# Optimization experiments

Hardware: AMD Instinct MI355X
Metric: run time of the kernel (lower is better)

## Reference

```python
import jax, jax.numpy as jnp
import numpy as np

HIDDEN = 1024
HEADS = 16
HEAD = HIDDEN // HEADS


def setup_inputs() -> dict:
    key = jax.random.key(0)
    ks = jax.random.split(key, 6)
    B, T = 2, 2048
    x = jax.random.normal(ks[0], (B, T, HIDDEN), dtype=jnp.float32)
    mask = jnp.ones((T, T), dtype=jnp.float32)
    s = 1.0 / np.sqrt(HIDDEN)
    Wqkv = jax.random.normal(ks[1], (HIDDEN, 3 * HIDDEN), dtype=jnp.float32) * s
    bqkv = jnp.zeros((3 * HIDDEN,), dtype=jnp.float32)
    Wproj = jax.random.normal(ks[2], (HIDDEN, HIDDEN), dtype=jnp.float32) * s
    bproj = jnp.zeros((HIDDEN,), dtype=jnp.float32)
    return {"x": x, "mask": mask, "Wqkv": Wqkv, "bqkv": bqkv,
            "Wproj": Wproj, "bproj": bproj}


def reference(x, mask, Wqkv, bqkv, Wproj, bproj):
    B, T, C = x.shape
    qkv = x @ Wqkv + bqkv                      # [B,T,3C]
    q, k, v = jnp.split(qkv, 3, axis=-1)
    def heads(t):                              # [B,T,C] -> [B,H,T,D]
        return t.reshape(B, T, HEADS, HEAD).transpose(0, 2, 1, 3)
    q, k, v = heads(q), heads(k), heads(v)
    scores = jnp.einsum('bhqd,bhkd->bhqk', q, k) / np.sqrt(HEAD)
    scores = jnp.where(mask == 0, -jnp.inf, scores)
    attn = jax.nn.softmax(scores, axis=-1)
    out = jnp.einsum('bhqk,bhkd->bhqd', attn, v)
    out = out.transpose(0, 2, 1, 3).reshape(B, T, C)
    return out @ Wproj + bproj
```

## Files before the change

kernel.cpp:

```cpp
#include <hip/hip_runtime.h>
#include <stdint.h>

#define HID 1024
#define NH 16
#define HD 64
#define BATCH 2
#define SEQ 2048
#define MR (BATCH*SEQ)
#define NQKV (3*HID)

typedef __attribute__((ext_vector_type(8))) _Float16 h16x8;
typedef __attribute__((ext_vector_type(2))) __fp16 fp16x2;
typedef __attribute__((ext_vector_type(8))) unsigned short u16x8;
typedef __attribute__((ext_vector_type(4))) float f32x4;

#if __has_builtin(__builtin_amdgcn_exp2f)
#define EXP2(x) __builtin_amdgcn_exp2f(x)
#else
#define EXP2(x) exp2f(x)
#endif

static __device__ __forceinline__ unsigned short f2h(float f) {
  union { _Float16 h; unsigned short u; } v; v.h = (_Float16)f; return v.u;
}
static __device__ __forceinline__ unsigned pk2(float a, float b) {
  union { fp16x2 h; unsigned u; } v;
  v.h = __builtin_amdgcn_cvt_pkrtz(a, b);
  return v.u;
}

typedef const __attribute__((address_space(1))) unsigned int glb_u32;
typedef __attribute__((address_space(3))) unsigned int lds_u32;
static __device__ __forceinline__ void cp16(const void* g, void* l) {
  __builtin_amdgcn_global_load_lds((glb_u32*)g, (lds_u32*)l, 16, 0, 0);
}

#define QSCL (0.125f * 1.44269504f)

__global__ __launch_bounds__(256) void k_cvt(const float4* __restrict__ src,
                                             ushort4* __restrict__ dst) {
  int i = blockIdx.x * 256 + threadIdx.x;
  float4 v = src[i];
  ushort4 h;
  h.x = f2h(v.x); h.y = f2h(v.y); h.z = f2h(v.z); h.w = f2h(v.w);
  dst[i] = h;
}

__global__ __launch_bounds__(256) void k_transpose_h(const float* __restrict__ src,
                                                     int R, int C,
                                                     unsigned short* __restrict__ dst) {
  __shared__ float tile[32][33];
  int tx = threadIdx.x, ty = threadIdx.y;
  int col0 = blockIdx.x * 32, row0 = blockIdx.y * 32;
  #pragma unroll
  for (int i = 0; i < 32; i += 8)
    tile[ty + i][tx] = src[(size_t)(row0 + ty + i) * C + col0 + tx];
  __syncthreads();
  #pragma unroll
  for (int i = 0; i < 32; i += 8) {
    float v = tile[tx][ty + i];
    dst[(size_t)(col0 + ty + i) * R + row0 + tx] = f2h(v);
  }
}

__global__ __launch_bounds__(256) void k_maskbits(const float* __restrict__ mask,
                                                  unsigned long long* __restrict__ mb) {
  int gw = blockIdx.x * 4 + (threadIdx.x >> 6);
  int lane = threadIdx.x & 63;
  float v = mask[(size_t)gw * 64 + lane];
  unsigned long long b = __ballot(v != 0.f);
  if (lane == 0) mb[gw] = b;
}

__global__ __launch_bounds__(256) void k_gemm_qkv(const unsigned short* __restrict__ A,
                                                  const unsigned short* __restrict__ Bt,
                                                  const float* __restrict__ bias,
                                                  unsigned short* __restrict__ Qp,
                                                  unsigned short* __restrict__ Kp,
                                                  unsigned short* __restrict__ Vt) {
  const int K = HID;
  int tid = threadIdx.x;
  int wave = tid >> 6, lane = tid & 63, quad = lane >> 4, l16 = lane & 15;
  int wm = wave >> 1, wn = wave & 1;
  int x7 = l16 & 7;
  int m0 = blockIdx.y * 128, n0 = blockIdx.x * 128;
  __shared__ __align__(16) unsigned short As[128 * 64], Bs[128 * 64];
  f32x4 acc[4][4] = {};
  for (int k0 = 0; k0 < K; k0 += 64) {
    __syncthreads();
    #pragma unroll
    for (int i = 0; i < 4; i++) {
      int c = tid + i * 256;
      int r = c >> 3, sc = ((c ^ r) & 7) << 3;
      cp16(&A[(size_t)(m0 + r) * K + k0 + sc], &As[c << 3]);
      cp16(&Bt[(size_t)(n0 + r) * K + k0 + sc], &Bs[c << 3]);
    }
    __syncthreads();
    #pragma unroll
    for (int kc = 0; kc < 2; kc++) {
      h16x8 af[4], bf[4];
      #pragma unroll
      for (int i = 0; i < 4; i++) {
        af[i] = *(const h16x8*)&As[(wm * 64 + i * 16 + l16) * 64 + (((kc * 4 + quad) ^ x7) << 3)];
        bf[i] = *(const h16x8*)&Bs[(wn * 64 + i * 16 + l16) * 64 + (((kc * 4 + quad) ^ x7) << 3)];
      }
      #pragma unroll
      for (int i = 0; i < 4; i++)
        #pragma unroll
        for (int j = 0; j < 4; j++)
          acc[i][j] = __builtin_amdgcn_mfma_f32_16x16x32_f16(af[i], bf[j], acc[i][j], 0, 0, 0);
    }
  }
  #pragma unroll
  for (int j = 0; j < 4; j++) {
    int n = n0 + wn * 64 + j * 16 + l16;
    float bv = bias[n];
    int which = n >> 10;
    int rem = n & 1023;
    int h = rem >> 6, d = rem & 63;
    if (which == 2) {
      #pragma unroll
      for (int i = 0; i < 4; i++) {
        int m = m0 + wm * 64 + i * 16 + quad * 4;
        int b = m >> 11, t = m & 2047;
        uint2 tt;
        tt.x = pk2(acc[i][j][0] + bv, acc[i][j][1] + bv);
        tt.y = pk2(acc[i][j][2] + bv, acc[i][j][3] + bv);
        *(uint2*)&Vt[(size_t)(b * NH + h) * (SEQ * HD) + (size_t)d * SEQ + t] = tt;
      }
    } else {
      #pragma unroll
      for (int i = 0; i < 4; i++)
        #pragma unroll
        for (int r = 0; r < 4; r++) {
          int m = m0 + wm * 64 + i * 16 + quad * 4 + r;
          int b = m >> 11, t = m & 2047;
          float val = acc[i][j][r] + bv;
          int hb = b * NH + h;
          if (which == 0) Qp[(size_t)hb * (SEQ * HD) + (size_t)t * HD + d] = f2h(val * QSCL);
          else            Kp[(size_t)hb * (SEQ * HD) + (size_t)t * HD + d] = f2h(val);
        }
    }
  }
}

__global__ __launch_bounds__(256) void k_attn(const unsigned short* __restrict__ Qp,
                                              const unsigned short* __restrict__ Kp,
                                              const unsigned short* __restrict__ Vt,
                                              const unsigned long long* __restrict__ mb,
                                              unsigned short* __restrict__ AO) {
  int tid = threadIdx.x, wave = tid >> 6, lane = tid & 63, quad = lane >> 4, l16 = lane & 15;
  int bh = blockIdx.y, qbase = blockIdx.x * 64;
  const unsigned short* Qg = Qp + (size_t)bh * (SEQ * HD);
  const unsigned short* Kg = Kp + (size_t)bh * (SEQ * HD);
  const unsigned short* Vg = Vt + (size_t)bh * (SEQ * HD);
  __shared__ __align__(16) unsigned short smem[16896];
  unsigned short* Qs = smem;
  unsigned short* Ks = smem + 4096;
  unsigned short* Vs = smem + 8192;
  unsigned short* Ps = smem + 12288 + wave * (16 * 72);
  unsigned short* Os = smem + 4096;

  #pragma unroll
  for (int i = 0; i < 2; i++) {
    int c = tid + i * 256;
    int row = c >> 3, sc = ((c ^ row) & 7) << 3;
    cp16(&Qg[(size_t)(qbase + row) * HD + sc], &Qs[c << 3]);
  }
  int qrow = qbase + wave * 16 + l16;
  const unsigned long long* mrow = mb + (size_t)qrow * 32;
  f32x4 acc_o[4] = {};
  f32x4 acc_l = {};
  int x7 = l16 & 7;

  h16x8 vone;
  #pragma unroll
  for (int j = 0; j < 8; j++) vone[j] = (_Float16)1.0f;

  __syncthreads();
  h16x8 bq[2];
  #pragma unroll
  for (int kk = 0; kk < 2; kk++)
    bq[kk] = *(const h16x8*)&Qs[(wave * 16 + l16) * 64 + (((kk * 4 + quad) ^ x7) << 3)];

  for (int kt = 0; kt < 32; kt++) {
    int kbase = kt * 64;
    __syncthreads();
    #pragma unroll
    for (int i = 0; i < 2; i++) {
      int c = tid + i * 256;
      int row = c >> 3, sc = ((c ^ row) & 7) << 3;
      cp16(&Kg[(size_t)(kbase + row) * HD + sc], &Ks[c << 3]);
      cp16(&Vg[(size_t)row * SEQ + kbase + sc], &Vs[c << 3]);
    }
    unsigned long long w = mrow[kt];
    __syncthreads();
    f32x4 s[4] = {};
    #pragma unroll
    for (int nt = 0; nt < 4; nt++)
      #pragma unroll
      for (int kk = 0; kk < 2; kk++) {
        h16x8 a = *(const h16x8*)&Ks[(nt * 16 + l16) * 64 + (((kk * 4 + quad) ^ x7) << 3)];
        s[nt] = __builtin_amdgcn_mfma_f32_16x16x32_f16(a, bq[kk], s[nt], 0, 0, 0);
      }
    if (!__all(w == ~0ULL)) {
      #pragma unroll
      for (int nt = 0; nt < 4; nt++)
        #pragma unroll
        for (int r = 0; r < 4; r++)
          if (!((w >> (nt * 16 + quad * 4 + r)) & 1ULL)) s[nt][r] = -100.f;
    }
    #pragma unroll
    for (int nt = 0; nt < 4; nt++)
      #pragma unroll
      for (int r = 0; r < 4; r++) s[nt][r] = EXP2(s[nt][r]);
    #pragma unroll
    for (int nt = 0; nt < 4; nt++) {
      uint2 t;
      t.x = pk2(s[nt][0], s[nt][1]);
      t.y = pk2(s[nt][2], s[nt][3]);
      *(uint2*)&Ps[l16 * 72 + nt * 16 + quad * 4] = t;
    }
    h16x8 bp[2];
    #pragma unroll
    for (int kk = 0; kk < 2; kk++)
      bp[kk] = *(const h16x8*)&Ps[l16 * 72 + kk * 32 + quad * 8];
    acc_l = __builtin_amdgcn_mfma_f32_16x16x32_f16(vone, bp[0], acc_l, 0, 0, 0);
    acc_l = __builtin_amdgcn_mfma_f32_16x16x32_f16(vone, bp[1], acc_l, 0, 0, 0);
    #pragma unroll
    for (int nt = 0; nt < 4; nt++)
      #pragma unroll
      for (int kk = 0; kk < 2; kk++) {
        h16x8 a = *(const h16x8*)&Vs[(nt * 16 + l16) * 64 + (((kk * 4 + quad) ^ x7) << 3)];
        acc_o[nt] = __builtin_amdgcn_mfma_f32_16x16x32_f16(a, bp[kk], acc_o[nt], 0, 0, 0);
      }
  }
  float rl = 1.0f / acc_l[0];
  __syncthreads();
  #pragma unroll
  for (int nt = 0; nt < 4; nt++) {
    uint2 t;
    t.x = (unsigned)f2h(acc_o[nt][0] * rl) | ((unsigned)f2h(acc_o[nt][1] * rl) << 16);
    t.y = (unsigned)f2h(acc_o[nt][2] * rl) | ((unsigned)f2h(acc_o[nt][3] * rl) << 16);
    *(uint2*)&Os[(wave * 16 + l16) * 72 + nt * 16 + quad * 4] = t;
  }
  __syncthreads();
  int b = bh >> 4, h = bh & 15;
  #pragma unroll
  for (int i = 0; i < 2; i++) {
    int c = tid + i * 256;
    int row = c >> 3, co = (c & 7) << 3;
    u16x8 vv = *(const u16x8*)&Os[row * 72 + co];
    *(u16x8*)&AO[(size_t)(b * SEQ + qbase + row) * HID + h * HD + co] = vv;
  }
}

__global__ __launch_bounds__(256) void k_gemm_proj(const unsigned short* __restrict__ A,
                                                   const unsigned short* __restrict__ Bt,
                                                   const float* __restrict__ bias,
                                                   float* __restrict__ out) {
  const int K = HID;
  int tid = threadIdx.x;
  int wave = tid >> 6, lane = tid & 63, quad = lane >> 4, l16 = lane & 15;
  int wm = wave >> 1, wn = wave & 1;
  int x7 = l16 & 7;
  int m0 = blockIdx.y * 128, n0 = blockIdx.x * 128;
  __shared__ __align__(16) unsigned short As[128 * 64], Bs[128 * 64];
  f32x4 acc[4][4] = {};
  for (int k0 = 0; k0 < K; k0 += 64) {
    __syncthreads();
    #pragma unroll
    for (int i = 0; i < 4; i++) {
      int c = tid + i * 256;
      int r = c >> 3, sc = ((c ^ r) & 7) << 3;
      cp16(&A[(size_t)(m0 + r) * K + k0 + sc], &As[c << 3]);
      cp16(&Bt[(size_t)(n0 + r) * K + k0 + sc], &Bs[c << 3]);
    }
    __syncthreads();
    #pragma unroll
    for (int kc = 0; kc < 2; kc++) {
      h16x8 af[4], bf[4];
      #pragma unroll
      for (int i = 0; i < 4; i++) {
        af[i] = *(const h16x8*)&As[(wm * 64 + i * 16 + l16) * 64 + (((kc * 4 + quad) ^ x7) << 3)];
        bf[i] = *(const h16x8*)&Bs[(wn * 64 + i * 16 + l16) * 64 + (((kc * 4 + quad) ^ x7) << 3)];
      }
      #pragma unroll
      for (int i = 0; i < 4; i++)
        #pragma unroll
        for (int j = 0; j < 4; j++)
          acc[i][j] = __builtin_amdgcn_mfma_f32_16x16x32_f16(af[i], bf[j], acc[i][j], 0, 0, 0);
    }
  }
  #pragma unroll
  for (int j = 0; j < 4; j++) {
    int n = n0 + wn * 64 + j * 16 + l16;
    float bv = bias[n];
    #pragma unroll
    for (int i = 0; i < 4; i++)
      #pragma unroll
      for (int r = 0; r < 4; r++) {
        int m = m0 + wm * 64 + i * 16 + quad * 4 + r;
        out[(size_t)m * HID + n] = acc[i][j][r] + bv;
      }
  }
}

extern "C" void kernel_launch(void* const* d_in, const int* in_sizes, int n_in,
                              void* d_out, int out_size, void* d_ws, size_t ws_size,
                              hipStream_t stream) {
  const float* x     = (const float*)d_in[0];
  const float* mask  = (const float*)d_in[1];
  const float* Wqkv  = (const float*)d_in[2];
  const float* bqkv  = (const float*)d_in[3];
  const float* Wproj = (const float*)d_in[4];
  const float* bproj = (const float*)d_in[5];
  float* out = (float*)d_out;

  uint8_t* ws = (uint8_t*)d_ws;
  size_t off = 0;
  auto alloc = [&](size_t bytes) -> void* {
    void* p = (void*)(ws + off);
    off += (bytes + 255) & ~(size_t)255;
    return p;
  };
  unsigned short* xh   = (unsigned short*)alloc((size_t)MR * HID * 2);
  unsigned short* WqT  = (unsigned short*)alloc((size_t)NQKV * HID * 2);
  unsigned short* WpT  = (unsigned short*)alloc((size_t)HID * HID * 2);
  unsigned short* Qp   = (unsigned short*)alloc((size_t)BATCH * NH * SEQ * HD * 2);
  unsigned short* Kp   = (unsigned short*)alloc((size_t)BATCH * NH * SEQ * HD * 2);
  unsigned short* Vtp  = (unsigned short*)alloc((size_t)BATCH * NH * SEQ * HD * 2);
  unsigned short* AO   = (unsigned short*)alloc((size_t)MR * HID * 2);
  unsigned long long* mb = (unsigned long long*)alloc((size_t)SEQ * (SEQ / 64) * 8);

  k_cvt<<<MR * HID / 4 / 256, 256, 0, stream>>>((const float4*)x, (ushort4*)xh);
  k_transpose_h<<<dim3(NQKV / 32, HID / 32), dim3(32, 8), 0, stream>>>(Wqkv, HID, NQKV, WqT);
  k_transpose_h<<<dim3(HID / 32, HID / 32), dim3(32, 8), 0, stream>>>(Wproj, HID, HID, WpT);
  k_maskbits<<<SEQ * (SEQ / 64) / 4, 256, 0, stream>>>(mask, mb);
  k_gemm_qkv<<<dim3(NQKV / 128, MR / 128), 256, 0, stream>>>(xh, WqT, bqkv, Qp, Kp, Vtp);
  k_attn<<<dim3(SEQ / 64, BATCH * NH), 256, 0, stream>>>(Qp, Kp, Vtp, mb, AO);
  k_gemm_proj<<<dim3(HID / 128, MR / 128), 256, 0, stream>>>(AO, WpT, bproj, out);
}
```

Baseline: 229.3 us.

## Double-buffer K/V in attention, fuse prep kernels, halve projection GEMM N-tile

Attention now prefetches the next K/V tile into a second LDS buffer while computing on the current one, leaving one barrier per iteration. The P and O scratch use XOR-swizzled 64-wide rows instead of padded ones. The four preprocessing kernels are merged into one launch, and the output projection uses 128x64 tiles to double the block count. The cost is more LDS per attention block, which may lower occupancy.

After: 226.5 us. No clear change (-1.2%).

```diff
diff --git a/kernel.cpp b/kernel.cpp
--- a/kernel.cpp
+++ b/kernel.cpp
@@ -37,39 +37,42 @@
 
 #define QSCL (0.125f * 1.44269504f)
 
-__global__ __launch_bounds__(256) void k_cvt(const float4* __restrict__ src,
-                                             ushort4* __restrict__ dst) {
-  int i = blockIdx.x * 256 + threadIdx.x;
-  float4 v = src[i];
-  ushort4 h;
-  h.x = f2h(v.x); h.y = f2h(v.y); h.z = f2h(v.z); h.w = f2h(v.w);
-  dst[i] = h;
-}
-
-__global__ __launch_bounds__(256) void k_transpose_h(const float* __restrict__ src,
-                                                     int R, int C,
-                                                     unsigned short* __restrict__ dst) {
+__global__ __launch_bounds__(256) void k_prep(const float4* __restrict__ x4,
+                                              const float* __restrict__ mask,
+                                              const float* __restrict__ Wqkv,
+                                              const float* __restrict__ Wproj,
+                                              ushort4* __restrict__ xh,
+                                              unsigned short* __restrict__ WqT,
+                                              unsigned short* __restrict__ WpT,
+                                              unsigned long long* __restrict__ mb) {
   __shared__ float tile[32][33];
-  int tx = threadIdx.x, ty = threadIdx.y;
-  int col0 = blockIdx.x * 32, row0 = blockIdx.y * 32;
-  #pragma unroll
-  for (int i = 0; i < 32; i += 8)
-    tile[ty + i][tx] = src[(size_t)(row0 + ty + i) * C + col0 + tx];
-  __syncthreads();
-  #pragma unroll
-  for (int i = 0; i < 32; i += 8) {
-    float v = tile[tx][ty + i];
-    dst[(size_t)(col0 + ty + i) * R + row0 + tx] = f2h(v);
-  }
-}
-
-__global__ __launch_bounds__(256) void k_maskbits(const float* __restrict__ mask,
-                                                  unsigned long long* __restrict__ mb) {
-  int gw = blockIdx.x * 4 + (threadIdx.x >> 6);
-  int lane = threadIdx.x & 63;
-  float v = mask[(size_t)gw * 64 + lane];
-  unsigned long long b = __ballot(v != 0.f);
-  if (lane == 0) mb[gw] = b;
+  int blk = blockIdx.x, tid = threadIdx.x;
+  if (blk < 4096) {
+    int i = blk * 256 + tid;
+    float4 v = x4[i];
+    ushort4 h;
+    h.x = f2h(v.x); h.y = f2h(v.y); h.z = f2h(v.z); h.w = f2h(v.w);
+    xh[i] = h;
+  } else if (blk < 8192) {
+    const float* src; unsigned short* dst; int C, bx, by;
+    if (blk < 7168) { src = Wqkv;  dst = WqT; C = NQKV; int b2 = blk - 4096; bx = b2 % 96; by = b2 / 96; }
+    else            { src = Wproj; dst = WpT; C = HID;  int b2 = blk - 7168; bx = b2 & 31; by = b2 >> 5; }
+    int tx = tid & 31, ty = tid >> 5;
+    int col0 = bx * 32, row0 = by * 32;
+    #pragma unroll
+    for (int i = 0; i < 32; i += 8)
+      tile[ty + i][tx] = src[(size_t)(row0 + ty + i) * C + col0 + tx];
+    __syncthreads();
+    #pragma unroll
+    for (int i = 0; i < 32; i += 8)
+      dst[(size_t)(col0 + ty + i) * HID + row0 + tx] = f2h(tile[tx][ty + i]);
+  } else {
+    int gw = (blk - 8192) * 4 + (tid >> 6);
+    int lane = tid & 63;
+    float v = mask[(size_t)gw * 64 + lane];
+    unsigned long long b = __ballot(v != 0.f);
+    if (lane == 0) mb[gw] = b;
+  }
 }
 
 __global__ __launch_bounds__(256) void k_gemm_qkv(const unsigned short* __restrict__ A,
@@ -154,11 +157,11 @@
   const unsigned short* Qg = Qp + (size_t)bh * (SEQ * HD);
   const unsigned short* Kg = Kp + (size_t)bh * (SEQ * HD);
   const unsigned short* Vg = Vt + (size_t)bh * (SEQ * HD);
-  __shared__ __align__(16) unsigned short smem[16896];
+  __shared__ __align__(16) unsigned short smem[20480];
   unsigned short* Qs = smem;
-  unsigned short* Ks = smem + 4096;
-  unsigned short* Vs = smem + 8192;
-  unsigned short* Ps = smem + 12288 + wave * (16 * 72);
+  unsigned short* Ksb = smem + 4096;
+  unsigned short* Vsb = smem + 12288;
+  unsigned short* Ps = smem + wave * 1024;
   unsigned short* Os = smem + 4096;
 
   #pragma unroll
@@ -166,6 +169,8 @@
     int c = tid + i * 256;
     int row = c >> 3, sc = ((c ^ row) & 7) << 3;
     cp16(&Qg[(size_t)(qbase + row) * HD + sc], &Qs[c << 3]);
+    cp16(&Kg[(size_t)row * HD + sc], &Ksb[c << 3]);
+    cp16(&Vg[(size_t)row * SEQ + sc], &Vsb[c << 3]);
   }
   int qrow = qbase + wave * 16 + l16;
   const unsigned long long* mrow = mb + (size_t)qrow * 32;
@@ -184,17 +189,22 @@
     bq[kk] = *(const h16x8*)&Qs[(wave * 16 + l16) * 64 + (((kk * 4 + quad) ^ x7) << 3)];
 
   for (int kt = 0; kt < 32; kt++) {
-    int kbase = kt * 64;
-    __syncthreads();
-    #pragma unroll
-    for (int i = 0; i < 2; i++) {
-      int c = tid + i * 256;
-      int row = c >> 3, sc = ((c ^ row) & 7) << 3;
-      cp16(&Kg[(size_t)(kbase + row) * HD + sc], &Ks[c << 3]);
-      cp16(&Vg[(size_t)row * SEQ + kbase + sc], &Vs[c << 3]);
+    int cur = kt & 1;
+    const unsigned short* Ks = Ksb + cur * 4096;
+    const unsigned short* Vs = Vsb + cur * 4096;
+    if (kt < 31) {
+      unsigned short* Kn = Ksb + (1 - cur) * 4096;
+      unsigned short* Vn = Vsb + (1 - cur) * 4096;
+      int kb1 = (kt + 1) * 64;
+      #pragma unroll
+      for (int i = 0; i < 2; i++) {
+        int c = tid + i * 256;
+        int row = c >> 3, sc = ((c ^ row) & 7) << 3;
+        cp16(&Kg[(size_t)(kb1 + row) * HD + sc], &Kn[c << 3]);
+        cp16(&Vg[(size_t)row * SEQ + kb1 + sc], &Vn[c << 3]);
+      }
     }
     unsigned long long w = mrow[kt];
-    __syncthreads();
     f32x4 s[4] = {};
     #pragma unroll
     for (int nt = 0; nt < 4; nt++)
@@ -219,12 +229,12 @@
       uint2 t;
       t.x = pk2(s[nt][0], s[nt][1]);
       t.y = pk2(s[nt][2], s[nt][3]);
-      *(uint2*)&Ps[l16 * 72 + nt * 16 + quad * 4] = t;
+      *(uint2*)&Ps[l16 * 64 + ((((nt * 2 + (quad >> 1)) ^ x7) << 3) | ((quad & 1) << 2))] = t;
     }
     h16x8 bp[2];
     #pragma unroll
     for (int kk = 0; kk < 2; kk++)
-      bp[kk] = *(const h16x8*)&Ps[l16 * 72 + kk * 32 + quad * 8];
+      bp[kk] = *(const h16x8*)&Ps[l16 * 64 + (((kk * 4 + quad) ^ x7) << 3)];
     acc_l = __builtin_amdgcn_mfma_f32_16x16x32_f16(vone, bp[0], acc_l, 0, 0, 0);
     acc_l = __builtin_amdgcn_mfma_f32_16x16x32_f16(vone, bp[1], acc_l, 0, 0, 0);
     #pragma unroll
@@ -234,24 +244,24 @@
         h16x8 a = *(const h16x8*)&Vs[(nt * 16 + l16) * 64 + (((kk * 4 + quad) ^ x7) << 3)];
         acc_o[nt] = __builtin_amdgcn_mfma_f32_16x16x32_f16(a, bp[kk], acc_o[nt], 0, 0, 0);
       }
+    __syncthreads();
   }
   float rl = 1.0f / acc_l[0];
-  __syncthreads();
   #pragma unroll
   for (int nt = 0; nt < 4; nt++) {
     uint2 t;
     t.x = (unsigned)f2h(acc_o[nt][0] * rl) | ((unsigned)f2h(acc_o[nt][1] * rl) << 16);
     t.y = (unsigned)f2h(acc_o[nt][2] * rl) | ((unsigned)f2h(acc_o[nt][3] * rl) << 16);
-    *(uint2*)&Os[(wave * 16 + l16) * 72 + nt * 16 + quad * 4] = t;
+    *(uint2*)&Os[(wave * 16 + l16) * 64 + ((((nt * 2 + (quad >> 1)) ^ x7) << 3) | ((quad & 1) << 2))] = t;
   }
   __syncthreads();
   int b = bh >> 4, h = bh & 15;
   #pragma unroll
   for (int i = 0; i < 2; i++) {
     int c = tid + i * 256;
-    int row = c >> 3, co = (c & 7) << 3;
-    u16x8 vv = *(const u16x8*)&Os[row * 72 + co];
-    *(u16x8*)&AO[(size_t)(b * SEQ + qbase + row) * HID + h * HD + co] = vv;
+    int row = c >> 3, j = c & 7;
+    u16x8 vv = *(const u16x8*)&Os[row * 64 + (((j ^ (row & 7)) << 3))];
+    *(u16x8*)&AO[(size_t)(b * SEQ + qbase + row) * HID + h * HD + (j << 3)] = vv;
   }
 }
 
@@ -264,9 +274,9 @@
   int wave = tid >> 6, lane = tid & 63, quad = lane >> 4, l16 = lane & 15;
   int wm = wave >> 1, wn = wave & 1;
   int x7 = l16 & 7;
-  int m0 = blockIdx.y * 128, n0 = blockIdx.x * 128;
-  __shared__ __align__(16) unsigned short As[128 * 64], Bs[128 * 64];
-  f32x4 acc[4][4] = {};
+  int m0 = blockIdx.y * 128, n0 = blockIdx.x * 64;
+  __shared__ __align__(16) unsigned short As[128 * 64], Bs[64 * 64];
+  f32x4 acc[4][2] = {};
   for (int k0 = 0; k0 < K; k0 += 64) {
     __syncthreads();
     #pragma unroll
@@ -274,27 +284,33 @@
       int c = tid + i * 256;
       int r = c >> 3, sc = ((c ^ r) & 7) << 3;
       cp16(&A[(size_t)(m0 + r) * K + k0 + sc], &As[c << 3]);
+    }
+    #pragma unroll
+    for (int i = 0; i < 2; i++) {
+      int c = tid + i * 256;
+      int r = c >> 3, sc = ((c ^ r) & 7) << 3;
       cp16(&Bt[(size_t)(n0 + r) * K + k0 + sc], &Bs[c << 3]);
     }
     __syncthreads();
     #pragma unroll
     for (int kc = 0; kc < 2; kc++) {
-      h16x8 af[4], bf[4];
-      #pragma unroll
-      for (int i = 0; i < 4; i++) {
+      h16x8 af[4], bf[2];
+      #pragma unroll
+      for (int i = 0; i < 4; i++)
         af[i] = *(const h16x8*)&As[(wm * 64 + i * 16 + l16) * 64 + (((kc * 4 + quad) ^ x7) << 3)];
-        bf[i] = *(const h16x8*)&Bs[(wn * 64 + i * 16 + l16) * 64 + (((kc * 4 + quad) ^ x7) << 3)];
-      }
+      #pragma unroll
+      for (int j = 0; j < 2; j++)
+        bf[j] = *(const h16x8*)&Bs[(wn * 32 + j * 16 + l16) * 64 + (((kc * 4 + quad) ^ x7) << 3)];
       #pragma unroll
       for (int i = 0; i < 4; i++)
         #pragma unroll
-        for (int j = 0; j < 4; j++)
+        for (int j = 0; j < 2; j++)
           acc[i][j] = __builtin_amdgcn_mfma_f32_16x16x32_f16(af[i], bf[j], acc[i][j], 0, 0, 0);
     }
   }
   #pragma unroll
-  for (int j = 0; j < 4; j++) {
-    int n = n0 + wn * 64 + j * 16 + l16;
+  for (int j = 0; j < 2; j++) {
+    int n = n0 + wn * 32 + j * 16 + l16;
     float bv = bias[n];
     #pragma unroll
     for (int i = 0; i < 4; i++)
@@ -333,11 +349,9 @@
   unsigned short* AO   = (unsigned short*)alloc((size_t)MR * HID * 2);
   unsigned long long* mb = (unsigned long long*)alloc((size_t)SEQ * (SEQ / 64) * 8);
 
-  k_cvt<<<MR * HID / 4 / 256, 256, 0, stream>>>((const float4*)x, (ushort4*)xh);
-  k_transpose_h<<<dim3(NQKV / 32, HID / 32), dim3(32, 8), 0, stream>>>(Wqkv, HID, NQKV, WqT);
-  k_transpose_h<<<dim3(HID / 32, HID / 32), dim3(32, 8), 0, stream>>>(Wproj, HID, HID, WpT);
-  k_maskbits<<<SEQ * (SEQ / 64) / 4, 256, 0, stream>>>(mask, mb);
+  k_prep<<<24576, 256, 0, stream>>>((const float4*)x, mask, Wqkv, Wproj,
+                                    (ushort4*)xh, WqT, WpT, mb);
   k_gemm_qkv<<<dim3(NQKV / 128, MR / 128), 256, 0, stream>>>(xh, WqT, bqkv, Qp, Kp, Vtp);
   k_attn<<<dim3(SEQ / 64, BATCH * NH), 256, 0, stream>>>(Qp, Kp, Vtp, mb, AO);
-  k_gemm_proj<<<dim3(HID / 128, MR / 128), 256, 0, stream>>>(AO, WpT, bproj, out);
-}
+  k_gemm_proj<<<dim3(HID / 64, MR / 128), 256, 0, stream>>>(AO, WpT, bproj, out);
+}
```
